# Optimization experiments

Hardware: AMD Instinct MI355X
Metric: run time of the kernel (lower is better)

## Reference

```python
import jax, jax.numpy as jnp
import numpy as np

N, C, H, W = 32, 512, 32, 32
D = C // 2  # theta/phi embed channels


def setup_inputs() -> dict:
    key = jax.random.key(0)
    ks = jax.random.split(key, 7)
    s = 0.05
    return {
        "x": jax.random.normal(ks[0], (N, C, H, W), jnp.float32),
        "W_theta": jax.random.normal(ks[1], (D, C), jnp.float32) * s,
        "b_theta": jax.random.normal(ks[2], (D,), jnp.float32) * s,
        "W_phi": jax.random.normal(ks[3], (D, C), jnp.float32) * s,
        "b_phi": jax.random.normal(ks[4], (D,), jnp.float32) * s,
        "W_fuse": jax.random.normal(ks[5], (C, C), jnp.float32) * s,
        "b_fuse": jax.random.normal(ks[6], (C,), jnp.float32) * s,
    }


def _conv1x1(x, Wt, bt):
    # 1x1 conv == per-pixel linear: [n,c,h,w] x [o,c] -> [n,o,h,w]
    return jnp.einsum('nchw,oc->nohw', x, Wt) + bt[None, :, None, None]


def reference(x, W_theta, b_theta, W_phi, b_phi, W_fuse, b_fuse):
    n, c, h, w = x.shape
    theta = _conv1x1(x, W_theta, b_theta)          # [n, d, h, w]
    phi = _conv1x1(x, W_phi, b_phi)                # [n, d, h, w]
    d = theta.shape[1]
    hw = h * w
    t = theta.reshape(n, d, hw)                    # queries [n, d, hw]
    p = phi.reshape(n, d, hw)                      # keys    [n, d, hw]
    g = x.reshape(n, c, hw)                        # values  [n, c, hw]
    scale = 1.0 / np.sqrt(float(d))
    f = jnp.einsum('ndq,ndk->nqk', t, p) * scale   # [n, hw, hw]
    f = jax.nn.softmax(f, axis=-1)
    attn = jnp.einsum('nqk,nck->ncq', f, g).reshape(n, c, h, w)
    return x + _conv1x1(attn, W_fuse, b_fuse)
```

## Files before the change

### kernel.cpp

```cpp
#include <hip/hip_runtime.h>


#define NB  32
#define CC  512
#define HWD 1024

typedef __attribute__((ext_vector_type(8))) short short8;
typedef __attribute__((ext_vector_type(4))) float f32x4;

__device__ __forceinline__ unsigned short f2bu(float f) {
    unsigned int u = __float_as_uint(f);
    u = (u + 0x7FFFu + ((u >> 16) & 1u)) >> 16;
    return (unsigned short)u;
}

__global__ __launch_bounds__(256) void k_packw(const float* __restrict__ Wt,
                                               const float* __restrict__ Wp,
                                               const float* __restrict__ Wf,
                                               unsigned short* __restrict__ Wcat,
                                               unsigned short* __restrict__ Wfuse) {
    int idx = blockIdx.x * 256 + threadIdx.x;
    int o = idx >> 9;
    float cv = (o < 256) ? Wt[idx] : Wp[idx - 131072];
    Wcat[idx]  = f2bu(cv);
    Wfuse[idx] = f2bu(Wf[idx]);
}

__global__ __launch_bounds__(512) void k_mm(const float* __restrict__ x,
                                            const unsigned short* __restrict__ Wcat,
                                            const unsigned short* __restrict__ Wfuse,
                                            const float* __restrict__ bt,
                                            const float* __restrict__ bp,
                                            unsigned short* __restrict__ tp,
                                            unsigned short* __restrict__ Z) {
    __shared__ __align__(16) float Tr[32 * 132];
    __shared__ __align__(16) unsigned short As[128 * 40];
    __shared__ __align__(16) unsigned short Bs[256 * 40];
    const int m0 = blockIdx.x << 7;
    const int yb = blockIdx.y;
    const bool isZ = (yb >= 2);
    const int n0 = (yb & 1) << 8;
    const unsigned short* W = isZ ? Wfuse : Wcat;
    const int n  = m0 >> 10, qbase = m0 & 1023;
    const int t = threadIdx.x, lane = t & 63, wave = t >> 6;
    const int wr = wave >> 2, wc = wave & 3;
    const int lrow = lane & 15, hi = lane >> 4, lhk = hi << 3;
    const f32x4 fz = {0.f, 0.f, 0.f, 0.f};
    f32x4 acc[4][4];
#pragma unroll
    for (int i = 0; i < 4; ++i)
#pragma unroll
        for (int j = 0; j < 4; ++j) acc[i][j] = fz;

    const int tr_r = t >> 4, tr_q = (t & 15) << 3;
    const int p2_pix = t & 127, p2_c = (t >> 7) << 3;

    for (int kt = 0; kt < 16; ++kt) {
        const int k0 = kt << 5;
        {
            const float* src = x + ((size_t)(n * CC + k0 + tr_r)) * HWD + qbase + tr_q;
            float4 v0 = *(const float4*)(src);
            float4 v1 = *(const float4*)(src + 4);
            *(float4*)(Tr + tr_r * 132 + tr_q) = v0;
            *(float4*)(Tr + tr_r * 132 + tr_q + 4) = v1;
#pragma unroll
            for (int i = 0; i < 2; ++i) {
                int chunk = t + (i << 9);
                int r = chunk >> 2, ko = (chunk & 3) << 3;
                *(uint4*)(Bs + r * 40 + ko) =
                    *(const uint4*)(W + ((size_t)(n0 + r)) * CC + k0 + ko);
            }
        }
        __syncthreads();
        {
            short8 o8;
#pragma unroll
            for (int j = 0; j < 8; ++j)
                o8[j] = (short)f2bu(Tr[(p2_c + j) * 132 + p2_pix]);
            *(short8*)(As + p2_pix * 40 + p2_c) = o8;
        }
        __syncthreads();
        short8 af[4], bfm[4];
#pragma unroll
        for (int mi = 0; mi < 4; ++mi)
            af[mi] = *(const short8*)(As + (wr * 64 + mi * 16 + lrow) * 40 + lhk);
#pragma unroll
        for (int ni = 0; ni < 4; ++ni)
            bfm[ni] = *(const short8*)(Bs + (wc * 64 + ni * 16 + lrow) * 40 + lhk);
#pragma unroll
        for (int mi = 0; mi < 4; ++mi)
#pragma unroll
            for (int ni = 0; ni < 4; ++ni)
                acc[mi][ni] = __builtin_amdgcn_mfma_f32_16x16x32_bf16(
                    af[mi], bfm[ni], acc[mi][ni], 0, 0, 0);
        __syncthreads();
    }
    if (!isZ) {
#pragma unroll
        for (int ni = 0; ni < 4; ++ni) {
            const int col = n0 + wc * 64 + ni * 16 + lrow;
            const float bias = (col < 256) ? bt[col] : bp[col - 256];
#pragma unroll
            for (int mi = 0; mi < 4; ++mi)
#pragma unroll
                for (int j = 0; j < 4; ++j) {
                    const int row = m0 + wr * 64 + mi * 16 + hi * 4 + j;
                    tp[(size_t)row * CC + col] = f2bu(acc[mi][ni][j] + bias);
                }
        }
    } else {
        const int kbase = qbase + wr * 64;
        unsigned short* Zn = Z + (size_t)n * CC * HWD;
#pragma unroll
        for (int ni = 0; ni < 4; ++ni) {
            const int o = n0 + wc * 64 + ni * 16 + lrow;
#pragma unroll
            for (int mi = 0; mi < 4; ++mi) {
                ushort4 v;
                v.x = f2bu(acc[mi][ni][0]);
                v.y = f2bu(acc[mi][ni][1]);
                v.z = f2bu(acc[mi][ni][2]);
                v.w = f2bu(acc[mi][ni][3]);
                *(ushort4*)(Zn + (size_t)o * HWD + kbase + mi * 16 + (hi << 2)) = v;
            }
        }
    }
}

__global__ __launch_bounds__(512, 2) void k_attn8(const unsigned short* __restrict__ tp,
                                                  const unsigned short* __restrict__ Z,
                                                  const float* __restrict__ bfu,
                                                  const float* __restrict__ x,
                                                  float* __restrict__ out) {
    constexpr int QST = 264;
    constexpr int PST = 264;
    constexpr int QSZ = 128 * QST;
    __shared__ __align__(16) unsigned short SL[QSZ + 128 * PST];
    __shared__ float rowsum[128];
    unsigned short* Qs = SL;
    unsigned short* P  = SL + QSZ;

    const int b = blockIdx.x;
    const int n = b & 31;
    const int q0 = (b >> 5) << 7;
    const int t = threadIdx.x, lane = t & 63, wave = t >> 6;
    const int lrow = lane & 15, hi = lane >> 4, lhk = hi << 3;
    const f32x4 fz = {0.f, 0.f, 0.f, 0.f};

    const unsigned short* tpn = tp + (size_t)n * HWD * CC;
    const unsigned short* Zn  = Z + (size_t)n * CC * HWD;

    if (t < 128) rowsum[t] = 0.f;
#pragma unroll
    for (int pass = 0; pass < 8; ++pass) {
        int chunk = (pass << 9) + t;
        int row = chunk >> 5, co = (chunk & 31) << 3;
        *(short8*)(Qs + row * QST + co) =
            *(const short8*)(tpn + (size_t)(q0 + row) * CC + co);
    }
    __syncthreads();

    f32x4 accG[8][4];
#pragma unroll
    for (int qj = 0; qj < 8; ++qj)
#pragma unroll
        for (int mi = 0; mi < 4; ++mi) accG[qj][mi] = fz;

    const int kw = wave << 4;
    const int ob = wave << 6;

    for (int it = 0; it < 4; ++it) {
        const int kv0 = it << 8;
        const size_t krow0 = (size_t)(kv0 + kw + lrow) * CC + 256;
        const size_t krow1 = (size_t)(kv0 + 128 + kw + lrow) * CC + 256;
        f32x4 accA[2][8];
#pragma unroll
        for (int k2 = 0; k2 < 2; ++k2)
#pragma unroll
            for (int qj = 0; qj < 8; ++qj) accA[k2][qj] = fz;
#pragma unroll
        for (int kt = 0; kt < 8; ++kt) {
            const int d0 = (kt << 5) + lhk;
            short8 kf0 = *(const short8*)(tpn + krow0 + d0);
            short8 kf1 = *(const short8*)(tpn + krow1 + d0);
#pragma unroll
            for (int qj = 0; qj < 8; ++qj) {
                short8 qfr = *(const short8*)(Qs + (qj * 16 + lrow) * QST + d0);
                accA[0][qj] = __builtin_amdgcn_mfma_f32_16x16x32_bf16(qfr, kf0, accA[0][qj], 0, 0, 0);
                accA[1][qj] = __builtin_amdgcn_mfma_f32_16x16x32_bf16(qfr, kf1, accA[1][qj], 0, 0, 0);
            }
        }
        float psum[8][4];
#pragma unroll
        for (int qj = 0; qj < 8; ++qj)
#pragma unroll
            for (int j = 0; j < 4; ++j) psum[qj][j] = 0.f;
#pragma unroll
        for (int k2 = 0; k2 < 2; ++k2) {
            const int pcol = (k2 << 7) + kw + lrow;
#pragma unroll
            for (int qj = 0; qj < 8; ++qj)
#pragma unroll
                for (int j = 0; j < 4; ++j) {
                    float p = __expf(accA[k2][qj][j] * 0.0625f);
                    psum[qj][j] += p;
                    P[(qj * 16 + hi * 4 + j) * PST + pcol] = f2bu(p);
                }
        }
#pragma unroll
        for (int qj = 0; qj < 8; ++qj)
#pragma unroll
            for (int j = 0; j < 4; ++j) {
                float s = psum[qj][j];
                s += __shfl_xor(s, 1, 16);
                s += __shfl_xor(s, 2, 16);
                s += __shfl_xor(s, 4, 16);
                s += __shfl_xor(s, 8, 16);
                if (lrow == 0) atomicAdd(&rowsum[qj * 16 + hi * 4 + j], s);
            }
        __syncthreads();
        __builtin_amdgcn_s_setprio(1);
#pragma unroll
        for (int ks = 0; ks < 8; ++ks) {
            const int kb = (ks << 5) + lhk;
            short8 zf[4];
#pragma unroll
            for (int mi = 0; mi < 4; ++mi)
                zf[mi] = *(const short8*)(Zn + (size_t)(ob + mi * 16 + lrow) * HWD + kv0 + kb);
#pragma unroll
            for (int qj = 0; qj < 8; ++qj) {
                short8 pa = *(const short8*)(P + (qj * 16 + lrow) * PST + kb);
#pragma unroll
                for (int mi = 0; mi < 4; ++mi)
                    accG[qj][mi] = __builtin_amdgcn_mfma_f32_16x16x32_bf16(
                        pa, zf[mi], accG[qj][mi], 0, 0, 0);
            }
        }
        __builtin_amdgcn_s_setprio(0);
        __syncthreads();
    }

    if (t < 128) rowsum[t] = 1.f / rowsum[t];
    __syncthreads();
    float bias[4];
#pragma unroll
    for (int mi = 0; mi < 4; ++mi) bias[mi] = bfu[ob + mi * 16 + lrow];
#pragma unroll
    for (int qj = 0; qj < 8; ++qj) {
        const float4 inv4 = *(const float4*)&rowsum[qj * 16 + (hi << 2)];
#pragma unroll
        for (int mi = 0; mi < 4; ++mi) {
            const int o = ob + mi * 16 + lrow;
            const size_t idx = ((size_t)(n * CC + o)) * HWD + q0 + qj * 16 + (hi << 2);
            const float4 xr = *(const float4*)(x + idx);
            float4 r;
            r.x = accG[qj][mi][0] * inv4.x + bias[mi] + xr.x;
            r.y = accG[qj][mi][1] * inv4.y + bias[mi] + xr.y;
            r.z = accG[qj][mi][2] * inv4.z + bias[mi] + xr.z;
            r.w = accG[qj][mi][3] * inv4.w + bias[mi] + xr.w;
            *(float4*)(out + idx) = r;
        }
    }
}

extern "C" void kernel_launch(void* const* d_in, const int* in_sizes, int n_in,
                              void* d_out, int out_size, void* d_ws, size_t ws_size,
                              hipStream_t stream) {
    const float* x  = (const float*)d_in[0];
    const float* Wt = (const float*)d_in[1];
    const float* bt = (const float*)d_in[2];
    const float* Wp = (const float*)d_in[3];
    const float* bp = (const float*)d_in[4];
    const float* Wf = (const float*)d_in[5];
    const float* bfu = (const float*)d_in[6];
    float* out = (float*)d_out;

    char* ws = (char*)d_ws;
    unsigned short* tp    = (unsigned short*)(ws);
    unsigned short* Z     = (unsigned short*)(ws + 33554432);
    unsigned short* Wcat  = (unsigned short*)(ws + 67108864);
    unsigned short* Wfuse = (unsigned short*)(ws + 67633152);

    k_packw<<<dim3(1024), 256, 0, stream>>>(Wt, Wp, Wf, Wcat, Wfuse);
    k_mm   <<<dim3(256, 4), 512, 0, stream>>>(x, Wcat, Wfuse, bt, bp, tp, Z);
    k_attn8<<<dim3(256), 512, 0, stream>>>(tp, Z, bfu, x, out);
}
```

Baseline: 170.4 us.

## Warp-specialize attention into producer score waves and consumer PV waves

The attention kernel now runs 768 threads split into two groups. Four waves compute QK^T scores and exp for half-tiles of 64 queries into a double-buffered P in shared memory. Eight waves consume the previous P buffer to accumulate P·Z, so score computation overlaps with the value GEMM. This adds a 9-stage barrier-synchronised pipeline and makes the producer waves recompute nothing but carry more key loads per half-tile. It risks register pressure under the 768-thread, 3-block launch bound and imbalance between the two wave groups.

New measurement: 257.6 us. 1.51x slower.

```diff
diff --git a/kernel.cpp b/kernel.cpp
--- a/kernel.cpp
+++ b/kernel.cpp
@@ -127,18 +127,19 @@
     }
 }
 
-__global__ __launch_bounds__(512, 2) void k_attn8(const unsigned short* __restrict__ tp,
-                                                  const unsigned short* __restrict__ Z,
-                                                  const float* __restrict__ bfu,
-                                                  const float* __restrict__ x,
-                                                  float* __restrict__ out) {
+__global__ __launch_bounds__(768, 3) void k_attn14(const unsigned short* __restrict__ tp,
+                                                   const unsigned short* __restrict__ Z,
+                                                   const float* __restrict__ bfu,
+                                                   const float* __restrict__ x,
+                                                   float* __restrict__ out) {
     constexpr int QST = 264;
     constexpr int PST = 264;
     constexpr int QSZ = 128 * QST;
-    __shared__ __align__(16) unsigned short SL[QSZ + 128 * PST];
+    constexpr int PHSZ = 64 * PST;
+    __shared__ __align__(16) unsigned short SL[QSZ + 2 * PHSZ];
     __shared__ float rowsum[128];
     unsigned short* Qs = SL;
-    unsigned short* P  = SL + QSZ;
+    unsigned short* Pbufs = SL + QSZ;
 
     const int b = blockIdx.x;
     const int n = b & 31;
@@ -151,114 +152,151 @@
     const unsigned short* Zn  = Z + (size_t)n * CC * HWD;
 
     if (t < 128) rowsum[t] = 0.f;
-#pragma unroll
-    for (int pass = 0; pass < 8; ++pass) {
-        int chunk = (pass << 9) + t;
-        int row = chunk >> 5, co = (chunk & 31) << 3;
-        *(short8*)(Qs + row * QST + co) =
-            *(const short8*)(tpn + (size_t)(q0 + row) * CC + co);
+    for (int pass = 0; pass < 6; ++pass) {
+        int chunk = pass * 768 + t;
+        if (chunk < 4096) {
+            int row = chunk >> 5, co = (chunk & 31) << 3;
+            *(short8*)(Qs + row * QST + co) =
+                *(const short8*)(tpn + (size_t)(q0 + row) * CC + co);
+        }
     }
     __syncthreads();
 
-    f32x4 accG[8][4];
-#pragma unroll
-    for (int qj = 0; qj < 8; ++qj)
-#pragma unroll
-        for (int mi = 0; mi < 4; ++mi) accG[qj][mi] = fz;
-
-    const int kw = wave << 4;
-    const int ob = wave << 6;
-
-    for (int it = 0; it < 4; ++it) {
-        const int kv0 = it << 8;
-        const size_t krow0 = (size_t)(kv0 + kw + lrow) * CC + 256;
-        const size_t krow1 = (size_t)(kv0 + 128 + kw + lrow) * CC + 256;
-        f32x4 accA[2][8];
-#pragma unroll
-        for (int k2 = 0; k2 < 2; ++k2)
-#pragma unroll
-            for (int qj = 0; qj < 8; ++qj) accA[k2][qj] = fz;
-#pragma unroll
-        for (int kt = 0; kt < 8; ++kt) {
-            const int d0 = (kt << 5) + lhk;
-            short8 kf0 = *(const short8*)(tpn + krow0 + d0);
-            short8 kf1 = *(const short8*)(tpn + krow1 + d0);
-#pragma unroll
-            for (int qj = 0; qj < 8; ++qj) {
-                short8 qfr = *(const short8*)(Qs + (qj * 16 + lrow) * QST + d0);
-                accA[0][qj] = __builtin_amdgcn_mfma_f32_16x16x32_bf16(qfr, kf0, accA[0][qj], 0, 0, 0);
-                accA[1][qj] = __builtin_amdgcn_mfma_f32_16x16x32_bf16(qfr, kf1, accA[1][qj], 0, 0, 0);
-            }
-        }
-        float psum[8][4];
+    if (wave < 4) {
+        const int ksb = wave << 6;
+        for (int s = 0; s < 9; ++s) {
+            if (s < 8) {
+                const int it = s >> 1, qh = s & 1;
+                const int kv0 = it << 8, qh0 = qh << 6;
+                unsigned short* Pb = Pbufs + (s & 1) * PHSZ;
+                f32x4 accA[4][4];
+#pragma unroll
+                for (int qj = 0; qj < 4; ++qj)
+#pragma unroll
+                    for (int kc = 0; kc < 4; ++kc) accA[qj][kc] = fz;
+#pragma unroll
+                for (int kt = 0; kt < 8; ++kt) {
+                    const int d0 = (kt << 5) + lhk;
+                    short8 kf[4];
+#pragma unroll
+                    for (int kc = 0; kc < 4; ++kc)
+                        kf[kc] = *(const short8*)(tpn +
+                            (size_t)(kv0 + ksb + kc * 16 + lrow) * CC + 256 + d0);
+#pragma unroll
+                    for (int qj = 0; qj < 4; ++qj) {
+                        short8 qfr = *(const short8*)(Qs + (qh0 + qj * 16 + lrow) * QST + d0);
+#pragma unroll
+                        for (int kc = 0; kc < 4; ++kc)
+                            accA[qj][kc] = __builtin_amdgcn_mfma_f32_16x16x32_bf16(
+                                qfr, kf[kc], accA[qj][kc], 0, 0, 0);
+                    }
+                }
+                float psum[4][4];
+#pragma unroll
+                for (int qj = 0; qj < 4; ++qj)
+#pragma unroll
+                    for (int j = 0; j < 4; ++j) psum[qj][j] = 0.f;
+#pragma unroll
+                for (int qj = 0; qj < 4; ++qj)
+#pragma unroll
+                    for (int kc = 0; kc < 4; ++kc)
+#pragma unroll
+                        for (int j = 0; j < 4; ++j) {
+                            float p = __expf(accA[qj][kc][j] * 0.0625f);
+                            psum[qj][j] += p;
+                            Pb[(qj * 16 + hi * 4 + j) * PST + ksb + kc * 16 + lrow] = f2bu(p);
+                        }
+#pragma unroll
+                for (int qj = 0; qj < 4; ++qj)
+#pragma unroll
+                    for (int j = 0; j < 4; ++j) {
+                        float sv = psum[qj][j];
+                        sv += __shfl_xor(sv, 1, 16);
+                        sv += __shfl_xor(sv, 2, 16);
+                        sv += __shfl_xor(sv, 4, 16);
+                        sv += __shfl_xor(sv, 8, 16);
+                        if (lrow == 0)
+                            atomicAdd(&rowsum[qh0 + qj * 16 + hi * 4 + j], sv);
+                    }
+            }
+            __syncthreads();
+        }
+    } else {
+        const int ob = (wave - 4) << 6;
+        f32x4 accG[8][4];
 #pragma unroll
         for (int qj = 0; qj < 8; ++qj)
 #pragma unroll
-            for (int j = 0; j < 4; ++j) psum[qj][j] = 0.f;
-#pragma unroll
-        for (int k2 = 0; k2 < 2; ++k2) {
-            const int pcol = (k2 << 7) + kw + lrow;
-#pragma unroll
-            for (int qj = 0; qj < 8; ++qj)
-#pragma unroll
-                for (int j = 0; j < 4; ++j) {
-                    float p = __expf(accA[k2][qj][j] * 0.0625f);
-                    psum[qj][j] += p;
-                    P[(qj * 16 + hi * 4 + j) * PST + pcol] = f2bu(p);
+            for (int mi = 0; mi < 4; ++mi) accG[qj][mi] = fz;
+
+        for (int s = 0; s < 9; ++s) {
+            if (s >= 1) {
+                const int sp = s - 1, it = sp >> 1;
+                const int kv0 = it << 8;
+                const unsigned short* Pb = Pbufs + (sp & 1) * PHSZ;
+                __builtin_amdgcn_s_setprio(1);
+                if ((sp & 1) == 0) {
+#pragma unroll
+                    for (int ks = 0; ks < 8; ++ks) {
+                        const int kb = (ks << 5) + lhk;
+                        short8 zf[4];
+#pragma unroll
+                        for (int mi = 0; mi < 4; ++mi)
+                            zf[mi] = *(const short8*)(Zn +
+                                (size_t)(ob + mi * 16 + lrow) * HWD + kv0 + kb);
+#pragma unroll
+                        for (int qjh = 0; qjh < 4; ++qjh) {
+                            short8 pa = *(const short8*)(Pb + (qjh * 16 + lrow) * PST + kb);
+#pragma unroll
+                            for (int mi = 0; mi < 4; ++mi)
+                                accG[qjh][mi] = __builtin_amdgcn_mfma_f32_16x16x32_bf16(
+                                    pa, zf[mi], accG[qjh][mi], 0, 0, 0);
+                        }
+                    }
+                } else {
+#pragma unroll
+                    for (int ks = 0; ks < 8; ++ks) {
+                        const int kb = (ks << 5) + lhk;
+                        short8 zf[4];
+#pragma unroll
+                        for (int mi = 0; mi < 4; ++mi)
+                            zf[mi] = *(const short8*)(Zn +
+                                (size_t)(ob + mi * 16 + lrow) * HWD + kv0 + kb);
+#pragma unroll
+                        for (int qjh = 0; qjh < 4; ++qjh) {
+                            short8 pa = *(const short8*)(Pb + (qjh * 16 + lrow) * PST + kb);
+#pragma unroll
+                            for (int mi = 0; mi < 4; ++mi)
+                                accG[4 + qjh][mi] = __builtin_amdgcn_mfma_f32_16x16x32_bf16(
+                                    pa, zf[mi], accG[4 + qjh][mi], 0, 0, 0);
+                        }
+                    }
                 }
-        }
-#pragma unroll
-        for (int qj = 0; qj < 8; ++qj)
-#pragma unroll
-            for (int j = 0; j < 4; ++j) {
-                float s = psum[qj][j];
-                s += __shfl_xor(s, 1, 16);
-                s += __shfl_xor(s, 2, 16);
-                s += __shfl_xor(s, 4, 16);
-                s += __shfl_xor(s, 8, 16);
-                if (lrow == 0) atomicAdd(&rowsum[qj * 16 + hi * 4 + j], s);
-            }
-        __syncthreads();
-        __builtin_amdgcn_s_setprio(1);
-#pragma unroll
-        for (int ks = 0; ks < 8; ++ks) {
-            const int kb = (ks << 5) + lhk;
-            short8 zf[4];
-#pragma unroll
-            for (int mi = 0; mi < 4; ++mi)
-                zf[mi] = *(const short8*)(Zn + (size_t)(ob + mi * 16 + lrow) * HWD + kv0 + kb);
-#pragma unroll
-            for (int qj = 0; qj < 8; ++qj) {
-                short8 pa = *(const short8*)(P + (qj * 16 + lrow) * PST + kb);
-#pragma unroll
-                for (int mi = 0; mi < 4; ++mi)
-                    accG[qj][mi] = __builtin_amdgcn_mfma_f32_16x16x32_bf16(
-                        pa, zf[mi], accG[qj][mi], 0, 0, 0);
-            }
-        }
-        __builtin_amdgcn_s_setprio(0);
-        __syncthreads();
-    }
-
-    if (t < 128) rowsum[t] = 1.f / rowsum[t];
-    __syncthreads();
-    float bias[4];
-#pragma unroll
-    for (int mi = 0; mi < 4; ++mi) bias[mi] = bfu[ob + mi * 16 + lrow];
-#pragma unroll
-    for (int qj = 0; qj < 8; ++qj) {
-        const float4 inv4 = *(const float4*)&rowsum[qj * 16 + (hi << 2)];
-#pragma unroll
-        for (int mi = 0; mi < 4; ++mi) {
-            const int o = ob + mi * 16 + lrow;
-            const size_t idx = ((size_t)(n * CC + o)) * HWD + q0 + qj * 16 + (hi << 2);
-            const float4 xr = *(const float4*)(x + idx);
-            float4 r;
-            r.x = accG[qj][mi][0] * inv4.x + bias[mi] + xr.x;
-            r.y = accG[qj][mi][1] * inv4.y + bias[mi] + xr.y;
-            r.z = accG[qj][mi][2] * inv4.z + bias[mi] + xr.z;
-            r.w = accG[qj][mi][3] * inv4.w + bias[mi] + xr.w;
-            *(float4*)(out + idx) = r;
+                __builtin_amdgcn_s_setprio(0);
+            }
+            __syncthreads();
+        }
+        float bias[4];
+#pragma unroll
+        for (int mi = 0; mi < 4; ++mi) bias[mi] = bfu[ob + mi * 16 + lrow];
+#pragma unroll
+        for (int qj = 0; qj < 8; ++qj) {
+            const float4 rs = *(const float4*)&rowsum[qj * 16 + (hi << 2)];
+            float4 inv4;
+            inv4.x = 1.f / rs.x; inv4.y = 1.f / rs.y;
+            inv4.z = 1.f / rs.z; inv4.w = 1.f / rs.w;
+#pragma unroll
+            for (int mi = 0; mi < 4; ++mi) {
+                const int o = ob + mi * 16 + lrow;
+                const size_t idx = ((size_t)(n * CC + o)) * HWD + q0 + qj * 16 + (hi << 2);
+                const float4 xr = *(const float4*)(x + idx);
+                float4 r;
+                r.x = accG[qj][mi][0] * inv4.x + bias[mi] + xr.x;
+                r.y = accG[qj][mi][1] * inv4.y + bias[mi] + xr.y;
+                r.z = accG[qj][mi][2] * inv4.z + bias[mi] + xr.z;
+                r.w = accG[qj][mi][3] * inv4.w + bias[mi] + xr.w;
+                *(float4*)(out + idx) = r;
+            }
         }
     }
 }
@@ -281,7 +319,7 @@
     unsigned short* Wcat  = (unsigned short*)(ws + 67108864);
     unsigned short* Wfuse = (unsigned short*)(ws + 67633152);
 
-    k_packw<<<dim3(1024), 256, 0, stream>>>(Wt, Wp, Wf, Wcat, Wfuse);
-    k_mm   <<<dim3(256, 4), 512, 0, stream>>>(x, Wcat, Wfuse, bt, bp, tp, Z);
-    k_attn8<<<dim3(256), 512, 0, stream>>>(tp, Z, bfu, x, out);
-}
+    k_packw <<<dim3(1024), 256, 0, stream>>>(Wt, Wp, Wf, Wcat, Wfuse);
+    k_mm    <<<dim3(256, 4), 512, 0, stream>>>(x, Wcat, Wfuse, bt, bp, tp, Z);
+    k_attn14<<<dim3(256), 768, 0, stream>>>(tp, Z, bfu, x, out);
+}
```
